# Kernel optimization log

Measured on AMD Instinct MI355X. Metric: run time of the kernel, lower is better.

Reference implementation:

```python
import jax, jax.numpy as jnp
import numpy as np

B, T, D, H = 2, 2048, 1024, 16
DH = D // H  # 64


def setup_inputs() -> dict:
    key = jax.random.key(0)
    ks = jax.random.split(key, 11)
    s = 1.0 / np.sqrt(D)
    return {
        "q": jax.random.normal(ks[0], (B, T, D), jnp.float32),
        "k": jax.random.normal(ks[1], (B, T, D), jnp.float32),
        "v": jax.random.normal(ks[2], (B, T, D), jnp.float32),
        "Wq": jax.random.normal(ks[3], (D, D), jnp.float32) * s,
        "bq": jnp.zeros((D,), jnp.float32),
        "Wk": jax.random.normal(ks[4], (D, D), jnp.float32) * s,
        "bk": jnp.zeros((D,), jnp.float32),
        "Wv": jax.random.normal(ks[5], (D, D), jnp.float32) * s,
        "bv": jnp.zeros((D,), jnp.float32),
        "Wo": jax.random.normal(ks[6], (D, D), jnp.float32) * s,
        "bo": jnp.zeros((D,), jnp.float32),
    }


def reference(q, k, v, Wq, bq, Wk, bk, Wv, bv, Wo, bo):
    Bq, Tq, _ = q.shape
    Tk = k.shape[1]
    # projections, split heads: [B, H, T, DH]
    qh = (q @ Wq + bq).reshape(Bq, Tq, H, DH).transpose(0, 2, 1, 3)
    kh = (k @ Wk + bk).reshape(Bq, Tk, H, DH).transpose(0, 2, 1, 3)
    vh = (v @ Wv + bv).reshape(Bq, Tk, H, DH).transpose(0, 2, 1, 3)
    # scores [B, H, Tq, Tk]
    scores = jnp.einsum("bhqd,bhkd->bhqk", qh, kh) / np.sqrt(DH)
    # causal mask with diagonal offset Tk - Tq (matches torch.tril semantics)
    ii = jnp.arange(Tq)[:, None]
    jj = jnp.arange(Tk)[None, :]
    causal = jj <= ii + (Tk - Tq)
    scores = jnp.where(causal, scores, -jnp.inf)
    attn = jax.nn.softmax(scores, axis=-1)
    x = jnp.einsum("bhqk,bhkd->bhqd", attn, vh)  # [B, H, Tq, DH]
    x = x.transpose(0, 2, 1, 3).reshape(Bq, Tq, H * DH)
    return x @ Wo + bo
```

## Files before the change

### kernel.cpp

```cpp
#include <hip/hip_runtime.h>

typedef unsigned short u16;
typedef unsigned int   u32;
typedef __attribute__((ext_vector_type(8)))  short short8;
typedef __attribute__((ext_vector_type(4)))  float f32x4;
typedef __attribute__((ext_vector_type(16))) float f32x16;
typedef __attribute__((ext_vector_type(2)))  u32 uint2v;
typedef __attribute__((ext_vector_type(4)))  u32 uint4v;

#define DEV __device__ __forceinline__

DEV u16 f2bf(float f) {
    u32 u = __builtin_bit_cast(u32, f);
    return (u16)((u + 0x7fffu + ((u >> 16) & 1u)) >> 16);
}
DEV float bf2f(u32 u) { return __builtin_bit_cast(float, u << 16); }
DEV u32 cvtpk(float a, float b) {
    u32 r;
    asm("v_cvt_pk_bf16_f32 %0, %1, %2" : "=v"(r) : "v"(a), "v"(b));
    return r;
}
typedef const __attribute__((address_space(1))) u32 g_u32;
typedef __attribute__((address_space(3))) u32 l_u32;
DEV void gload16(const u16* g, u16* l) {
    __builtin_amdgcn_global_load_lds((g_u32*)g, (l_u32*)l, 16, 0, 0);
}


template<int OMODE>
DEV void gemm_body(const u16* __restrict__ A_, const u16* __restrict__ Bt,
                   const float* __restrict__ bias, float oscale, void* C_) {
    constexpr int Kd = 1024;
    const int m0 = blockIdx.y * 128, n0 = blockIdx.x * 128;
    const int t = threadIdx.x, lane = t & 63, w = t >> 6;
    const int wm = w >> 1, wn = w & 1;
    const int l15 = lane & 15, l4 = lane >> 4;
    __shared__ __align__(16) u16 As[128 * 32];
    __shared__ __align__(16) u16 Bs[128 * 32];
    f32x4 acc[4][4] = {};

    for (int k0 = 0; k0 < Kd; k0 += 32) {
        #pragma unroll
        for (int rnd = 0; rnd < 2; rnd++) {
            int cc = rnd * 256 + t, row = cc >> 2, slot = cc & 3;
            gload16(Bt + (size_t)(n0 + row) * Kd + k0 + slot * 8, Bs + cc * 8);
            gload16(A_ + (size_t)(m0 + row) * Kd + k0 + slot * 8, As + cc * 8);
        }
        __syncthreads();
        short8 af[4], bfr[4];
        #pragma unroll
        for (int i = 0; i < 4; i++) {
            af[i]  = *(const short8*)(As + (wm * 64 + i * 16 + l15) * 32 + l4 * 8);
            bfr[i] = *(const short8*)(Bs + (wn * 64 + i * 16 + l15) * 32 + l4 * 8);
        }
        #pragma unroll
        for (int i = 0; i < 4; i++)
            #pragma unroll
            for (int j = 0; j < 4; j++)
                acc[i][j] = __builtin_amdgcn_mfma_f32_16x16x32_bf16(af[i], bfr[j], acc[i][j], 0, 0, 0);
        __syncthreads();
    }

    #pragma unroll
    for (int i = 0; i < 4; i++) {
        #pragma unroll
        for (int j = 0; j < 4; j++) {
            int col = n0 + wn * 64 + j * 16 + l15;
            int mb  = m0 + wm * 64 + i * 16 + l4 * 4;
            float bv = bias[col];
            if (OMODE == 2) {
                float* C = (float*)C_;
                #pragma unroll
                for (int r = 0; r < 4; r++)
                    C[(size_t)(mb + r) * 1024 + col] = acc[i][j][r] + bv;
            } else if (OMODE == 0) {
                u16* C = (u16*)C_;
                #pragma unroll
                for (int r = 0; r < 4; r++)
                    C[(size_t)(mb + r) * 1024 + col] = f2bf((acc[i][j][r] + bv) * oscale);
            } else if (OMODE == 3) {
                u16* C = (u16*)C_;
                int hh = col >> 6, dd = col & 63;
                int bb = mb >> 11, tt = mb & 2047;
                size_t tile = ((size_t)(bb * 16 + hh) * 64 + (tt >> 5)) * 2048;
                int c = dd >> 4, hi2 = (dd >> 3) & 1, e = dd & 7;
                int lob = tt & 31;
                #pragma unroll
                for (int r = 0; r < 4; r++)
                    C[tile + (size_t)((c * 2 + hi2) * 32 + lob + r) * 8 + e] =
                        f2bf(acc[i][j][r] + bv);
            } else {
                u16* C = (u16*)C_;
                int hh = col >> 6, dd = col & 63;
                int bb = mb >> 11, tt = mb & 2047;
                size_t tile = ((size_t)(bb * 16 + hh) * 64 + (tt >> 5)) * 2048;
                int tin = tt & 31, kc = tin >> 4, hi2 = (tin >> 3) & 1, e0 = tin & 7;
                int c2 = dd >> 5, lo2 = dd & 31;
                size_t off = tile + (size_t)((kc * 2 + c2) * 64 + hi2 * 32 + lo2) * 8 + e0;
                uint2v pp;
                pp[0] = cvtpk(acc[i][j][0] + bv, acc[i][j][1] + bv);
                pp[1] = cvtpk(acc[i][j][2] + bv, acc[i][j][3] + bv);
                *(uint2v*)(C + off) = pp;
            }
        }
    }
}

__global__ __launch_bounds__(256) void k_transw(const float* Wq, const float* Wk,
                                                const float* Wv, const float* Wo, u16* Wt) {
    int z = blockIdx.z;
    const float* W = z == 0 ? Wq : z == 1 ? Wk : z == 2 ? Wv : Wo;
    u16* O = Wt + (size_t)z * 1048576;
    __shared__ float tile[32][33];
    int n0 = blockIdx.x * 32, k0 = blockIdx.y * 32;
    int tx = threadIdx.x, ty = threadIdx.y;
    #pragma unroll
    for (int i = 0; i < 32; i += 8) tile[ty + i][tx] = W[(size_t)(k0 + ty + i) * 1024 + n0 + tx];
    __syncthreads();
    #pragma unroll
    for (int i = 0; i < 32; i += 8) O[(size_t)(n0 + ty + i) * 1024 + k0 + tx] = f2bf(tile[tx][ty + i]);
}

__global__ __launch_bounds__(256) void k_cvt(const float* q, const float* k, const float* v,
                                             u16* Abf) {
    int z = blockIdx.z;
    const float* src = z == 0 ? q : z == 1 ? k : v;
    u16* dst = Abf + (size_t)z * 4194304;
    size_t i = ((size_t)blockIdx.x * 256 + threadIdx.x) * 8;
    float4 a = *(const float4*)(src + i);
    float4 b = *(const float4*)(src + i + 4);
    uint4v o;
    o[0] = cvtpk(a.x, a.y); o[1] = cvtpk(a.z, a.w);
    o[2] = cvtpk(b.x, b.y); o[3] = cvtpk(b.z, b.w);
    *(uint4v*)(dst + i) = o;
}

__global__ __launch_bounds__(256) void k_proj(const u16* Abf, const u16* Wt,
                                              const float* bq, const float* bk,
                                              const float* bv, u16* QKV) {
    int z = blockIdx.z;
    if (z == 2)
        gemm_body<1>(Abf + (size_t)2 * 4194304, Wt + (size_t)2 * 1048576, bv, 1.f,
                     QKV + (size_t)2 * 4194304);
    else if (z == 1)
        gemm_body<3>(Abf + (size_t)4194304, Wt + (size_t)1048576, bk, 1.f,
                     QKV + (size_t)4194304);
    else
        gemm_body<0>(Abf, Wt, bq, 0.125f * 1.44269504088896f, QKV);
}

__global__ __launch_bounds__(256) void k_gemm_out(const u16* Xc, const u16* Wt,
                                                  const float* bo, float* out) {
    gemm_body<2>(Xc, Wt, bo, 1.f, out);
}

__global__ __launch_bounds__(256, 2) void k_attn(const u16* __restrict__ Qp,
                                                 const u16* __restrict__ Kp2,
                                                 const u16* __restrict__ Vp2,
                                                 u16* __restrict__ Xc) {
    const int bh = blockIdx.y, b = bh >> 4, h = bh & 15;
    const int t = threadIdx.x, lane = t & 63, w = t >> 6;
    const int lo = lane & 31, hi = lane >> 5;
    const int j = 15 - (int)blockIdx.x;
    const int q0 = (j * 4 + w) * 32;
    const int NTw = j * 4 + w + 1;
    const int NT  = j * 4 + 4;
    const u16* Qb = Qp + (size_t)(b * 2048) * 1024 + h * 64;
    const u16* Kb = Kp2 + (size_t)bh * 64 * 2048;
    const u16* Vb = Vp2 + (size_t)bh * 64 * 2048;

    __shared__ __align__(16) u16 Ks[2][2048];
    __shared__ __align__(16) u16 Vs[2][2048];

    short8 qf[4];
    #pragma unroll
    for (int c = 0; c < 4; c++)
        qf[c] = *(const short8*)(Qb + (size_t)(q0 + lo) * 1024 + c * 16 + hi * 8);

    f32x16 O0 = {}, O1 = {};
    float lsum = 0.f;
    const int qg = q0 + lo;

#define STAGE(buf, kt) do {                                                              \
        gload16(Kb + (size_t)(kt) * 2048 + t * 8, Ks[buf] + t * 8);                      \
        gload16(Vb + (size_t)(kt) * 2048 + t * 8, Vs[buf] + t * 8);                      \
    } while (0)

    STAGE(0, 0);
    for (int kt = 0; kt < NT; kt++) {
        __syncthreads();
        if (kt + 1 < NT) STAGE((kt + 1) & 1, kt + 1);
        if (kt < NTw) {
            const u16* kl = Ks[kt & 1];
            const u16* vl = Vs[kt & 1];
            short8 kf[4], vf[4];
            #pragma unroll
            for (int c = 0; c < 4; c++) {
                kf[c] = *(const short8*)(kl + (c * 64 + lane) * 8);
                vf[c] = *(const short8*)(vl + (c * 64 + lane) * 8);
            }
            f32x16 S = {};
            #pragma unroll
            for (int c = 0; c < 4; c++)
                S = __builtin_amdgcn_mfma_f32_32x32x16_bf16(kf[c], qf[c], S, 0, 0, 0);
            const bool diag = (kt == NTw - 1);
            #pragma unroll
            for (int kc = 0; kc < 2; kc++) {
                float pv[8];
                #pragma unroll
                for (int jj = 0; jj < 8; jj++) {
                    int r = kc * 8 + jj;
                    float s = S[r];
                    if (diag) {
                        int kg = kt * 32 + (r & 3) + 8 * (r >> 2) + 4 * hi;
                        s = (kg <= qg) ? s : -1e30f;
                    }
                    pv[jj] = __builtin_amdgcn_exp2f(s);
                }
                lsum += (((pv[0] + pv[1]) + (pv[2] + pv[3])) +
                         ((pv[4] + pv[5]) + (pv[6] + pv[7])));
                u32 w0 = cvtpk(pv[0], pv[1]), w1 = cvtpk(pv[2], pv[3]);
                u32 w2 = cvtpk(pv[4], pv[5]), w3 = cvtpk(pv[6], pv[7]);
                auto r0 = __builtin_amdgcn_permlane32_swap(w0, w2, false, false);
                auto r1 = __builtin_amdgcn_permlane32_swap(w1, w3, false, false);
                uint4v fw; fw[0] = r0[0]; fw[1] = r1[0]; fw[2] = r0[1]; fw[3] = r1[1];
                short8 pf = __builtin_bit_cast(short8, fw);
                O0 = __builtin_amdgcn_mfma_f32_32x32x16_bf16(pf, vf[kc * 2 + 0], O0, 0, 0, 0);
                O1 = __builtin_amdgcn_mfma_f32_32x32x16_bf16(pf, vf[kc * 2 + 1], O1, 0, 0, 0);
            }
        }
    }
#undef STAGE

    float ltot = lsum + __shfl_xor(lsum, 32, 64);
    #pragma unroll
    for (int r = 0; r < 16; r++) {
        int qr = (r & 3) + 8 * (r >> 2) + 4 * hi;
        float lt = __shfl(ltot, qr, 64);
        float linv = lt > 0.f ? 1.f / lt : 0.f;
        size_t rowb = (size_t)(b * 2048 + q0 + qr) * 1024 + h * 64;
        Xc[rowb + lo]      = f2bf(O0[r] * linv);
        Xc[rowb + 32 + lo] = f2bf(O1[r] * linv);
    }
}

extern "C" void kernel_launch(void* const* d_in, const int* in_sizes, int n_in,
                              void* d_out, int out_size, void* d_ws, size_t ws_size,
                              hipStream_t stream) {
    (void)in_sizes; (void)n_in; (void)out_size; (void)ws_size;
    const float* q  = (const float*)d_in[0];
    const float* k  = (const float*)d_in[1];
    const float* v  = (const float*)d_in[2];
    const float* Wq = (const float*)d_in[3];
    const float* bq = (const float*)d_in[4];
    const float* Wk = (const float*)d_in[5];
    const float* bk = (const float*)d_in[6];
    const float* Wv = (const float*)d_in[7];
    const float* bv = (const float*)d_in[8];
    const float* Wo = (const float*)d_in[9];
    const float* bo = (const float*)d_in[10];

    u16* Wt  = (u16*)d_ws;
    u16* QKV = Wt + (size_t)4 * 1048576;
    u16* Abf = QKV + (size_t)3 * 4194304;
    u16* Xc  = Abf;

    k_transw<<<dim3(32, 32, 4), dim3(32, 8), 0, stream>>>(Wq, Wk, Wv, Wo, Wt);
    k_cvt<<<dim3(2048, 1, 3), 256, 0, stream>>>(q, k, v, Abf);
    k_proj<<<dim3(8, 32, 3), 256, 0, stream>>>(Abf, Wt, bq, bk, bv, QKV);
    k_attn<<<dim3(16, 32), 256, 0, stream>>>(QKV, QKV + (size_t)4194304,
                                             QKV + (size_t)2 * 4194304, Xc);
    k_gemm_out<<<dim3(8, 32), 256, 0, stream>>>(Xc, Wt + (size_t)3 * 1048576,
                                                bo, (float*)d_out);
}
```

Before: 143.0 us.

## Split attention KV loop into two parity partitions with combine kernel

The attention kernel now launches twice as many blocks. Each block processes only the even or the odd key tiles, writes a partially normalized output plus its row sum, and a new combine kernel merges the two partials by their softmax sums. This is meant to raise occupancy and parallelism on the long causal rows, which had too few blocks in flight. The cost is an extra kernel launch, more traffic for the partial buffers, and an extra bf16 rounding step. Because the softmax uses no running max, the partials can be merged simply by their sums.

```diff
diff --git a/kernel.cpp b/kernel.cpp
--- a/kernel.cpp
+++ b/kernel.cpp
@@ -149,6 +149,26 @@
         gemm_body<0>(Abf, Wt, bq, 0.125f * 1.44269504088896f, QKV);
 }
 
+__global__ __launch_bounds__(256) void k_combine(const u16* Xp, const float* Lp, u16* Xc) {
+    size_t idx = (size_t)blockIdx.x * 256 + threadIdx.x;
+    size_t e = idx * 8;
+    int row = (int)(e >> 10), hh = ((int)e & 1023) >> 6;
+    float l0 = Lp[(size_t)row * 16 + hh];
+    float l1 = Lp[65536 + (size_t)row * 16 + hh];
+    float s = 1.0f / (l0 + l1);
+    float w0 = l0 * s, w1 = l1 * s;
+    uint4v x0 = *(const uint4v*)(Xp + e);
+    uint4v x1 = *(const uint4v*)(Xp + (size_t)4194304 + e);
+    uint4v o;
+    #pragma unroll
+    for (int j = 0; j < 4; j++) {
+        float a0 = bf2f(x0[j] & 0xffffu) * w0 + bf2f(x1[j] & 0xffffu) * w1;
+        float a1 = bf2f(x0[j] >> 16)    * w0 + bf2f(x1[j] >> 16)    * w1;
+        o[j] = cvtpk(a0, a1);
+    }
+    *(uint4v*)(Xc + e) = o;
+}
+
 __global__ __launch_bounds__(256) void k_gemm_out(const u16* Xc, const u16* Wt,
                                                   const float* bo, float* out) {
     gemm_body<2>(Xc, Wt, bo, 1.f, out);
@@ -157,14 +177,15 @@
 __global__ __launch_bounds__(256, 2) void k_attn(const u16* __restrict__ Qp,
                                                  const u16* __restrict__ Kp2,
                                                  const u16* __restrict__ Vp2,
-                                                 u16* __restrict__ Xc) {
+                                                 u16* __restrict__ Xp, float* __restrict__ Lp) {
     const int bh = blockIdx.y, b = bh >> 4, h = bh & 15;
     const int t = threadIdx.x, lane = t & 63, w = t >> 6;
     const int lo = lane & 31, hi = lane >> 5;
+    const int par = blockIdx.z;
     const int j = 15 - (int)blockIdx.x;
     const int q0 = (j * 4 + w) * 32;
     const int NTw = j * 4 + w + 1;
-    const int NT  = j * 4 + 4;
+    const int NPH = 2 * j + 2;
     const u16* Qb = Qp + (size_t)(b * 2048) * 1024 + h * 64;
     const u16* Kb = Kp2 + (size_t)bh * 64 * 2048;
     const u16* Vb = Vp2 + (size_t)bh * 64 * 2048;
@@ -186,13 +207,14 @@
         gload16(Vb + (size_t)(kt) * 2048 + t * 8, Vs[buf] + t * 8);                      \
     } while (0)
 
-    STAGE(0, 0);
-    for (int kt = 0; kt < NT; kt++) {
+    STAGE(0, par);
+    for (int i = 0; i < NPH; i++) {
         __syncthreads();
-        if (kt + 1 < NT) STAGE((kt + 1) & 1, kt + 1);
+        if (i + 1 < NPH) STAGE((i + 1) & 1, 2 * (i + 1) + par);
+        const int kt = 2 * i + par;
         if (kt < NTw) {
-            const u16* kl = Ks[kt & 1];
-            const u16* vl = Vs[kt & 1];
+            const u16* kl = Ks[i & 1];
+            const u16* vl = Vs[i & 1];
             short8 kf[4], vf[4];
             #pragma unroll
             for (int c = 0; c < 4; c++) {
@@ -233,15 +255,18 @@
 #undef STAGE
 
     float ltot = lsum + __shfl_xor(lsum, 32, 64);
+    u16* Xb = Xp + (size_t)par * 4194304;
     #pragma unroll
     for (int r = 0; r < 16; r++) {
         int qr = (r & 3) + 8 * (r >> 2) + 4 * hi;
         float lt = __shfl(ltot, qr, 64);
         float linv = lt > 0.f ? 1.f / lt : 0.f;
         size_t rowb = (size_t)(b * 2048 + q0 + qr) * 1024 + h * 64;
-        Xc[rowb + lo]      = f2bf(O0[r] * linv);
-        Xc[rowb + 32 + lo] = f2bf(O1[r] * linv);
-    }
+        Xb[rowb + lo]      = f2bf(O0[r] * linv);
+        Xb[rowb + 32 + lo] = f2bf(O1[r] * linv);
+    }
+    if (hi == 0)
+        Lp[(size_t)par * 65536 + (size_t)(b * 2048 + q0 + lo) * 16 + h] = ltot;
 }
 
 extern "C" void kernel_launch(void* const* d_in, const int* in_sizes, int n_in,
@@ -260,16 +285,19 @@
     const float* Wo = (const float*)d_in[9];
     const float* bo = (const float*)d_in[10];
 
-    u16* Wt  = (u16*)d_ws;
-    u16* QKV = Wt + (size_t)4 * 1048576;
-    u16* Abf = QKV + (size_t)3 * 4194304;
-    u16* Xc  = Abf;
+    u16*   Wt  = (u16*)d_ws;
+    u16*   QKV = Wt + (size_t)4 * 1048576;
+    u16*   Abf = QKV + (size_t)3 * 4194304;
+    u16*   Xp  = Abf;
+    u16*   Xc  = Abf + (size_t)2 * 4194304;
+    float* Lp  = (float*)(Abf + (size_t)3 * 4194304);
 
     k_transw<<<dim3(32, 32, 4), dim3(32, 8), 0, stream>>>(Wq, Wk, Wv, Wo, Wt);
     k_cvt<<<dim3(2048, 1, 3), 256, 0, stream>>>(q, k, v, Abf);
     k_proj<<<dim3(8, 32, 3), 256, 0, stream>>>(Abf, Wt, bq, bk, bv, QKV);
-    k_attn<<<dim3(16, 32), 256, 0, stream>>>(QKV, QKV + (size_t)4194304,
-                                             QKV + (size_t)2 * 4194304, Xc);
+    k_attn<<<dim3(16, 32, 2), 256, 0, stream>>>(QKV, QKV + (size_t)4194304,
+                                                QKV + (size_t)2 * 4194304, Xp, Lp);
+    k_combine<<<2048, 256, 0, stream>>>(Xp, Lp, Xc);
     k_gemm_out<<<dim3(8, 32), 256, 0, stream>>>(Xc, Wt + (size_t)3 * 1048576,
                                                 bo, (float*)d_out);
 }
```

New measurement: 136.5 us. 4.5% less time.
